# Performance work log

Measured on AMD Instinct MI355X. Metric: run time of the kernel, lower is better.

The kernel has to match this reference:

```python
import jax, jax.numpy as jnp
import numpy as np

LMAX = 4  # number of l blocks (lmax+1 in the original)
# segment ids mapping the L2 = sum(2l+1) = 16 spherical components to their l block
SEG = np.repeat(np.arange(LMAX), 2 * np.arange(LMAX) + 1)  # [16]
SEG_ONEHOT = np.eye(LMAX, dtype=np.float32)[SEG]  # [16, LMAX]


def setup_inputs() -> dict:
    key = jax.random.key(0)
    ks = jax.random.split(key, 10)
    b, m, f, k, L2 = 16, 64, 128, 64, 16
    def rnd(kk, shape, scale):
        return jax.random.normal(kk, shape, dtype=jnp.float32) * scale
    return {
        'x': rnd(ks[0], (b, m, f, L2), 1.0),
        'y': rnd(ks[1], (b, m, f, L2), 1.0),
        'wx0': rnd(ks[2], (k, f, f, LMAX), 1.0 / np.sqrt(f * f * LMAX)),
        'wy0': rnd(ks[3], (k, f, f, LMAX), 1.0 / np.sqrt(f * f * LMAX)),
        'wx_mlp': rnd(ks[4], (2, k, k), 1.0 / np.sqrt(k)),
        'bx_mlp': rnd(ks[5], (2, k, k), 0.02),
        'wy_mlp': rnd(ks[6], (2, k, k), 1.0 / np.sqrt(k)),
        'by_mlp': rnd(ks[7], (2, k, k), 0.02),
        'wxf': rnd(ks[8], (LMAX, f, k), 1.0 / np.sqrt(k)),
        'wyf': rnd(ks[9], (LMAX, f, k), 1.0 / np.sqrt(k)),
    }


def reference(x, y, wx0, wy0, wx_mlp, bx_mlp, wy_mlp, by_mlp, wxf, wyf):
    act = jax.nn.silu
    S = jnp.asarray(SEG_ONEHOT)  # [L2, lmax]
    # outer product of y and x features, segment-summed over each l block:
    # mix[b,m,fy,fx,l] = sum_c y[b,m,fy,c] * x[b,m,fx,c] * S[c,l]
    mix = jnp.einsum('bmfc,bmgc,cl->bmfgl', y, x, S)  # [b,m,f,f,lmax]
    mx = jnp.einsum('bmfgl,kfgl->bmk', mix, wx0)
    my = jnp.einsum('bmfgl,kfgl->bmk', mix, wy0)
    for i in range(wx_mlp.shape[0]):  # the n_mlp-1 used MLP stages
        mx = act(jnp.einsum('bmk,kl->bml', mx, wx_mlp[i]) + bx_mlp[i])
        my = act(jnp.einsum('bmk,kl->bml', my, wy_mlp[i]) + by_mlp[i])
    mx = act(jnp.einsum('bmk,lfk->bmfl', mx, wxf))  # [b,m,f,lmax]
    my = act(jnp.einsum('bmk,lfk->bmfl', my, wyf))
    # broadcast each l gate over its 2l+1 components (repeat == gather by SEG)
    seg = jnp.asarray(SEG)
    res = mx[..., seg] * x + my[..., seg] * y  # [b,m,f,L2]
    return res
```

## Files before the change

kernel.cpp:

```cpp
#include <hip/hip_runtime.h>
#include <stdint.h>


#define AS1 __attribute__((address_space(1)))
#define AS3 __attribute__((address_space(3)))

typedef __bf16 bf16x8 __attribute__((ext_vector_type(8)));
typedef float f32x4 __attribute__((ext_vector_type(4)));

__device__ __forceinline__ uint16_t f2b(float f) {
  uint32_t u = __float_as_uint(f);
  u += 0x7fffu + ((u >> 16) & 1u);
  return (uint16_t)(u >> 16);
}

#if __has_builtin(__builtin_amdgcn_fdot2_f32_bf16)
typedef __bf16 bf16x2 __attribute__((ext_vector_type(2)));
__device__ __forceinline__ float dot2b(uint32_t a, uint32_t b, float c) {
  union { uint32_t u; bf16x2 v; } ua, ub;
  ua.u = a; ub.u = b;
  return __builtin_amdgcn_fdot2_f32_bf16(ua.v, ub.v, c, false);
}
#else
__device__ __forceinline__ float dot2b(uint32_t a, uint32_t b, float c) {
  float a0 = __uint_as_float(a << 16), a1 = __uint_as_float(a & 0xffff0000u);
  float b0 = __uint_as_float(b << 16), b1 = __uint_as_float(b & 0xffff0000u);
  return c + a0 * b0 + a1 * b1;
}
#endif

__global__ __launch_bounds__(256) void convert_all(
    const float* __restrict__ wx0, const float* __restrict__ wy0,
    const float* __restrict__ x, const float* __restrict__ y,
    const float* __restrict__ wxf, const float* __restrict__ wyf,
    uint16_t* __restrict__ Wb, uint16_t* __restrict__ xb,
    uint16_t* __restrict__ yb, float* __restrict__ wfT) {
  if (blockIdx.x >= 6144) {
    int base = (blockIdx.x - 6144) * 2048 + threadIdx.x * 8;
#pragma unroll
    for (int ii = 0; ii < 8; ++ii) {
      int idx = base + ii;
      int side = idx >> 15, rem = idx & 32767;
      int k = rem >> 9, l = (rem >> 7) & 3, f = rem & 127;
      const float* src = side ? wyf : wxf;
      wfT[idx] = src[((size_t)l * 128 + f) * 64 + k];
    }
    return;
  }
  size_t i = ((size_t)blockIdx.x * 256 + threadIdx.x) * 8;
  const float* s; uint16_t* d;
  if (i < 4194304)        { s = wx0 + i;              d = Wb + i; }
  else if (i < 8388608)   { s = wy0 + (i - 4194304);  d = Wb + i; }
  else if (i < 10485760)  { s = x + (i - 8388608);    d = xb + (i - 8388608); }
  else                    { s = y + (i - 10485760);   d = yb + (i - 10485760); }
  float4 v0 = *(const float4*)s;
  float4 v1 = *(const float4*)(s + 4);
  uint32_t o0 = (uint32_t)f2b(v0.x) | ((uint32_t)f2b(v0.y) << 16);
  uint32_t o1 = (uint32_t)f2b(v0.z) | ((uint32_t)f2b(v0.w) << 16);
  uint32_t o2 = (uint32_t)f2b(v1.x) | ((uint32_t)f2b(v1.y) << 16);
  uint32_t o3 = (uint32_t)f2b(v1.z) | ((uint32_t)f2b(v1.w) << 16);
  *(uint4*)d = make_uint4(o0, o1, o2, o3);
}

__device__ __forceinline__ void gload_lds16(const void* g, void* l) {
  __builtin_amdgcn_global_load_lds((const AS1 uint32_t*)g, (AS3 uint32_t*)l, 16, 0, 0);
}

__global__ __launch_bounds__(256, 3) void fused_gemm(
    const uint16_t* __restrict__ xb, const uint16_t* __restrict__ yb,
    const uint16_t* __restrict__ Wb, float* __restrict__ Cpart) {
  __shared__ __align__(16) uint16_t sA[2][128 * 40];
  __shared__ __align__(16) uint16_t sB[2][128 * 32];
  __shared__ __align__(16) uint16_t yS[2][2048];

  int tid = threadIdx.x;
  int w = tid >> 6, lane = tid & 63;
  int g_id = blockIdx.x;
  int fb = g_id >> 3, fyg = g_id & 7;
  int FB = fb * 8;
  int fy0 = fyg * 16;
  int m0 = blockIdx.y * 128;
  int r = lane & 15, q = lane >> 4;
  int wm = w >> 1, wn = w & 1;
  int rowl = lane >> 2, qq = lane & 3;
  int m_loc = tid & 127, half = tid >> 7;

  uint32_t xr[32];
  {
    const uint16_t* xp0 = xb + (size_t)(m0 + m_loc) * 2048 + (FB + half * 4) * 16;
#pragma unroll
    for (int j = 0; j < 8; ++j) {
      uint4 v = *(const uint4*)(xp0 + j * 8);
      xr[j * 4 + 0] = v.x; xr[j * 4 + 1] = v.y;
      xr[j * 4 + 2] = v.z; xr[j * 4 + 3] = v.w;
    }
  }

  f32x4 zero = {0.f, 0.f, 0.f, 0.f};
  f32x4 acc[4][4];
#pragma unroll
  for (int i = 0; i < 4; ++i)
#pragma unroll
    for (int j = 0; j < 4; ++j) acc[i][j] = zero;

  int bcol = qq ^ ((rowl >> 1) & 3);
  int ychunk = w >> 1, ymbase = (w & 1) * 64;
  const uint16_t* ysrc_base = yb + (size_t)(m0 + ymbase + lane) * 2048 + ychunk * 8;
  int ydst_off = ychunk * 1024 + ymbase * 8;

  auto issueB = [&](uint16_t* dstB, int t) {
    int kk0 = (fy0 + t) * 512 + FB * 4;
#pragma unroll
    for (int jj = 0; jj < 2; ++jj) {
      int blk = w * 2 + jj;
      int rowi = blk * 16 + rowl;
      gload_lds16(Wb + (size_t)rowi * 65536 + kk0 + bcol * 8, dstB + blk * 512);
    }
  };
  auto issueY = [&](uint16_t* dstY, int t) {
    gload_lds16(ysrc_base + (size_t)(fy0 + t) * 16, dstY + ydst_off);
  };
  auto computeG = [&](const uint16_t* srcY, float* gg) {
    uint4 ya = *(const uint4*)(srcY + m_loc * 8);
    uint4 yc = *(const uint4*)(srcY + 1024 + m_loc * 8);
    uint32_t yp[8] = {ya.x, ya.y, ya.z, ya.w, yc.x, yc.y, yc.z, yc.w};
    uint32_t yl0 = yp[0] & 0xffffu, yh0 = yp[0] & 0xffff0000u;
    uint32_t yl4 = yp[4] & 0xffffu, yh4 = yp[4] & 0xffff0000u;
#pragma unroll
    for (int fxp = 0; fxp < 4; ++fxp) {
      const uint32_t* xp = xr + fxp * 8;
      gg[fxp * 4 + 0] = dot2b(xp[0], yl0, 0.f);
      gg[fxp * 4 + 1] = dot2b(xp[1], yp[1], dot2b(xp[0], yh0, 0.f));
      gg[fxp * 4 + 2] = dot2b(xp[4], yl4,
                         dot2b(xp[3], yp[3], dot2b(xp[2], yp[2], 0.f)));
      gg[fxp * 4 + 3] = dot2b(xp[7], yp[7], dot2b(xp[6], yp[6],
                         dot2b(xp[5], yp[5], dot2b(xp[4], yh4, 0.f))));
    }
  };
  auto writeA = [&](uint16_t* dstA, const float* gg) {
    uint32_t o[8];
#pragma unroll
    for (int p = 0; p < 8; ++p)
      o[p] = (__float_as_uint(gg[2 * p]) >> 16) |
             (__float_as_uint(gg[2 * p + 1]) & 0xffff0000u);
    uint16_t* dst = dstA + m_loc * 40 + half * 16;
    *(uint4*)dst       = make_uint4(o[0], o[1], o[2], o[3]);
    *(uint4*)(dst + 8) = make_uint4(o[4], o[5], o[6], o[7]);
  };

  uint16_t *pAc = sA[0], *pAn = sA[1];
  uint16_t *pBc = sB[0], *pBn = sB[1];
  uint16_t *pYc = yS[0], *pYn = yS[1];

  float gg[16];
  issueY(pYc, 0);
  __syncthreads();
  computeG(pYc, gg);
  writeA(pAc, gg);
  issueB(pBc, 0);
  issueY(pYn, 1);
  __syncthreads();

  for (int t = 0; t < 16; ++t) {
    if (t < 15) {
      issueB(pBn, t + 1);
      if (t < 14) issueY(pYc, t + 2);
      computeG(pYn, gg);
      writeA(pAn, gg);
    }
    bf16x8 a[4], b[4];
#pragma unroll
    for (int i = 0; i < 4; ++i)
      a[i] = *(const bf16x8*)&pAc[(wm * 64 + i * 16 + r) * 40 + q * 8];
#pragma unroll
    for (int j = 0; j < 4; ++j) {
      int row = wn * 64 + j * 16 + r;
      int pos = q ^ ((row >> 1) & 3);
      b[j] = *(const bf16x8*)&pBc[row * 32 + pos * 8];
    }
#pragma unroll
    for (int i = 0; i < 4; ++i)
#pragma unroll
      for (int j = 0; j < 4; ++j)
        acc[i][j] = __builtin_amdgcn_mfma_f32_16x16x32_bf16(a[i], b[j], acc[i][j], 0, 0, 0);
    __syncthreads();
    uint16_t* tp;
    tp = pAc; pAc = pAn; pAn = tp;
    tp = pBc; pBc = pBn; pBn = tp;
    tp = pYc; pYc = pYn; pYn = tp;
  }

  float* cbase = Cpart + (size_t)g_id * 131072;
#pragma unroll
  for (int i = 0; i < 4; ++i)
#pragma unroll
    for (int j = 0; j < 4; ++j)
#pragma unroll
      for (int reg = 0; reg < 4; ++reg) {
        int mm = m0 + wm * 64 + i * 16 + q * 4 + reg;
        int nn = wn * 64 + j * 16 + r;
        cbase[(size_t)mm * 128 + nn] = acc[i][j][reg];
      }
}

__global__ __launch_bounds__(256) void reduce_kernel(
    const float* __restrict__ Cpart, float* __restrict__ Cred) {
  __shared__ float sred[256];
  int t = threadIdx.x, bm = blockIdx.x;
  int col = t & 127, hh = t >> 7;
  float s = 0.f;
#pragma unroll 8
  for (int sp = hh * 64; sp < hh * 64 + 64; ++sp)
    s += Cpart[(size_t)sp * 131072 + (size_t)bm * 128 + col];
  sred[t] = s;
  __syncthreads();
  if (t < 128) Cred[(size_t)bm * 128 + t] = sred[t] + sred[t + 128];
}

__global__ __launch_bounds__(256) void finish_kernel(
    const float* __restrict__ x, const float* __restrict__ y,
    const float* __restrict__ wx_mlp, const float* __restrict__ bx_mlp,
    const float* __restrict__ wy_mlp, const float* __restrict__ by_mlp,
    const float* __restrict__ wfT,
    const float* __restrict__ Cred, float* __restrict__ out) {
  const int seg[16] = {0,1,1,1,2,2,2,2,2,3,3,3,3,3,3,3};
  __shared__ float sm[128];
  __shared__ float sg[2][128][4];
  int t = threadIdx.x;
  int bm = blockIdx.x;
  int mi = bm & 63;

  if (t < 128) sm[t] = Cred[(size_t)bm * 128 + t];
  __syncthreads();

  for (int st = 0; st < 2; ++st) {
    float v = 0.f;
    if (t < 128) {
      int side = t >> 6, j = t & 63;
      const float* wmlp = side ? wy_mlp : wx_mlp;
      const float* bmlp = side ? by_mlp : bx_mlp;
      const float* mv = sm + side * 64;
#pragma unroll 8
      for (int k = 0; k < 64; ++k)
        v += mv[k] * wmlp[(st * 64 + k) * 64 + j];
      v += bmlp[(st * 64 + mi) * 64 + j];
      v = v / (1.f + __expf(-v));
    }
    __syncthreads();
    if (t < 128) sm[t] = v;
    __syncthreads();
  }

  {
    int side = t >> 7, f = t & 127;
    const float* base = wfT + side * 32768;
    const float* mv = sm + side * 64;
    float gg[4] = {0.f, 0.f, 0.f, 0.f};
#pragma unroll 8
    for (int k = 0; k < 64; ++k) {
      float m2 = mv[k];
#pragma unroll
      for (int l = 0; l < 4; ++l)
        gg[l] += m2 * base[(k * 4 + l) * 128 + f];
    }
#pragma unroll
    for (int l = 0; l < 4; ++l)
      sg[side][f][l] = gg[l] / (1.f + __expf(-gg[l]));
  }
  __syncthreads();

  {
    int f = t >> 1, half = t & 1;
    size_t base = ((size_t)bm * 128 + f) * 16 + half * 8;
    float4 xa = *(const float4*)(x + base), xb4 = *(const float4*)(x + base + 4);
    float4 ya = *(const float4*)(y + base), yb4 = *(const float4*)(y + base + 4);
    float xv[8] = {xa.x, xa.y, xa.z, xa.w, xb4.x, xb4.y, xb4.z, xb4.w};
    float yv[8] = {ya.x, ya.y, ya.z, ya.w, yb4.x, yb4.y, yb4.z, yb4.w};
    float o[8];
#pragma unroll
    for (int ii = 0; ii < 8; ++ii) {
      int c = half * 8 + ii;
      o[ii] = sg[0][f][seg[c]] * xv[ii] + sg[1][f][seg[c]] * yv[ii];
    }
    *(float4*)(out + base)     = make_float4(o[0], o[1], o[2], o[3]);
    *(float4*)(out + base + 4) = make_float4(o[4], o[5], o[6], o[7]);
  }
}

extern "C" void kernel_launch(void* const* d_in, const int* in_sizes, int n_in,
                              void* d_out, int out_size, void* d_ws, size_t ws_size,
                              hipStream_t stream) {
  const float* x      = (const float*)d_in[0];
  const float* y      = (const float*)d_in[1];
  const float* wx0    = (const float*)d_in[2];
  const float* wy0    = (const float*)d_in[3];
  const float* wx_mlp = (const float*)d_in[4];
  const float* bx_mlp = (const float*)d_in[5];
  const float* wy_mlp = (const float*)d_in[6];
  const float* by_mlp = (const float*)d_in[7];
  const float* wxf    = (const float*)d_in[8];
  const float* wyf    = (const float*)d_in[9];
  float* out = (float*)d_out;

  uint16_t* Wb    = (uint16_t*)d_ws;
  uint16_t* xb    = (uint16_t*)((char*)d_ws + (size_t)16777216);
  uint16_t* yb    = (uint16_t*)((char*)d_ws + (size_t)20971520);
  float*    Cpart = (float*)((char*)d_ws + (size_t)25165824);
  float*    wfT   = (float*)((char*)d_ws + (size_t)92274688);
  float*    Cred  = (float*)((char*)d_ws + (size_t)92536832);

  convert_all<<<6176, 256, 0, stream>>>(wx0, wy0, x, y, wxf, wyf, Wb, xb, yb, wfT);
  fused_gemm<<<dim3(128, 8), 256, 0, stream>>>(xb, yb, Wb, Cpart);
  reduce_kernel<<<1024, 256, 0, stream>>>(Cpart, Cred);
  finish_kernel<<<1024, 256, 0, stream>>>(x, y, wx_mlp, bx_mlp, wy_mlp, by_mlp,
                                          wfT, Cred, out);
}
```

Before: 183.2 us.

## Keep x/y in fp32, transpose y, store bf16 partials, fold reduce into finish

Removes the bf16 conversion of x and y; instead y is transposed in fp32 so each fy slice is contiguous, and the mix products are computed in fp32 FMAs before a rounded bf16 pack. GEMM split-K partials are stored as bf16 instead of fp32, halving that traffic. The separate reduce kernel is merged into the finish kernel, saving a launch and the Cred round trip. The trade-offs are more VGPRs for the fp32 x registers, a larger y LDS buffer, and lower precision in the partial sums.

```diff
diff --git a/kernel.cpp b/kernel.cpp
--- a/kernel.cpp
+++ b/kernel.cpp
@@ -13,30 +13,36 @@
   u += 0x7fffu + ((u >> 16) & 1u);
   return (uint16_t)(u >> 16);
 }
-
-#if __has_builtin(__builtin_amdgcn_fdot2_f32_bf16)
-typedef __bf16 bf16x2 __attribute__((ext_vector_type(2)));
-__device__ __forceinline__ float dot2b(uint32_t a, uint32_t b, float c) {
-  union { uint32_t u; bf16x2 v; } ua, ub;
-  ua.u = a; ub.u = b;
-  return __builtin_amdgcn_fdot2_f32_bf16(ua.v, ub.v, c, false);
-}
-#else
-__device__ __forceinline__ float dot2b(uint32_t a, uint32_t b, float c) {
-  float a0 = __uint_as_float(a << 16), a1 = __uint_as_float(a & 0xffff0000u);
-  float b0 = __uint_as_float(b << 16), b1 = __uint_as_float(b & 0xffff0000u);
-  return c + a0 * b0 + a1 * b1;
-}
-#endif
+__device__ __forceinline__ float b2f(uint16_t u) {
+  return __uint_as_float((uint32_t)u << 16);
+}
 
 __global__ __launch_bounds__(256) void convert_all(
     const float* __restrict__ wx0, const float* __restrict__ wy0,
-    const float* __restrict__ x, const float* __restrict__ y,
+    const float* __restrict__ y,
     const float* __restrict__ wxf, const float* __restrict__ wyf,
-    uint16_t* __restrict__ Wb, uint16_t* __restrict__ xb,
-    uint16_t* __restrict__ yb, float* __restrict__ wfT) {
-  if (blockIdx.x >= 6144) {
-    int base = (blockIdx.x - 6144) * 2048 + threadIdx.x * 8;
+    uint16_t* __restrict__ Wb, float* __restrict__ yT,
+    float* __restrict__ wfT) {
+  if (blockIdx.x < 4096) {
+    size_t i = ((size_t)blockIdx.x * 256 + threadIdx.x) * 8;
+    const float* s = (i < 4194304) ? (wx0 + i) : (wy0 + (i - 4194304));
+    float4 v0 = *(const float4*)s;
+    float4 v1 = *(const float4*)(s + 4);
+    uint32_t o0 = (uint32_t)f2b(v0.x) | ((uint32_t)f2b(v0.y) << 16);
+    uint32_t o1 = (uint32_t)f2b(v0.z) | ((uint32_t)f2b(v0.w) << 16);
+    uint32_t o2 = (uint32_t)f2b(v1.x) | ((uint32_t)f2b(v1.y) << 16);
+    uint32_t o3 = (uint32_t)f2b(v1.z) | ((uint32_t)f2b(v1.w) << 16);
+    *(uint4*)(Wb + i) = make_uint4(o0, o1, o2, o3);
+  } else if (blockIdx.x < 4608) {
+    int g = (blockIdx.x - 4096) * 256 + threadIdx.x;
+    int m = g >> 7, fy = g & 127;
+    const float* src = y + (size_t)m * 2048 + fy * 16;
+    float* dst = yT + (size_t)fy * 16384 + m * 16;
+#pragma unroll
+    for (int ii = 0; ii < 4; ++ii)
+      *(float4*)(dst + ii * 4) = *(const float4*)(src + ii * 4);
+  } else {
+    int base = (blockIdx.x - 4608) * 2048 + threadIdx.x * 8;
 #pragma unroll
     for (int ii = 0; ii < 8; ++ii) {
       int idx = base + ii;
@@ -45,21 +51,7 @@
       const float* src = side ? wyf : wxf;
       wfT[idx] = src[((size_t)l * 128 + f) * 64 + k];
     }
-    return;
-  }
-  size_t i = ((size_t)blockIdx.x * 256 + threadIdx.x) * 8;
-  const float* s; uint16_t* d;
-  if (i < 4194304)        { s = wx0 + i;              d = Wb + i; }
-  else if (i < 8388608)   { s = wy0 + (i - 4194304);  d = Wb + i; }
-  else if (i < 10485760)  { s = x + (i - 8388608);    d = xb + (i - 8388608); }
-  else                    { s = y + (i - 10485760);   d = yb + (i - 10485760); }
-  float4 v0 = *(const float4*)s;
-  float4 v1 = *(const float4*)(s + 4);
-  uint32_t o0 = (uint32_t)f2b(v0.x) | ((uint32_t)f2b(v0.y) << 16);
-  uint32_t o1 = (uint32_t)f2b(v0.z) | ((uint32_t)f2b(v0.w) << 16);
-  uint32_t o2 = (uint32_t)f2b(v1.x) | ((uint32_t)f2b(v1.y) << 16);
-  uint32_t o3 = (uint32_t)f2b(v1.z) | ((uint32_t)f2b(v1.w) << 16);
-  *(uint4*)d = make_uint4(o0, o1, o2, o3);
+  }
 }
 
 __device__ __forceinline__ void gload_lds16(const void* g, void* l) {
@@ -67,11 +59,12 @@
 }
 
 __global__ __launch_bounds__(256, 3) void fused_gemm(
-    const uint16_t* __restrict__ xb, const uint16_t* __restrict__ yb,
-    const uint16_t* __restrict__ Wb, float* __restrict__ Cpart) {
+    const float* __restrict__ x, const float* __restrict__ yT,
+    const uint16_t* __restrict__ Wb, uint16_t* __restrict__ Cpart) {
   __shared__ __align__(16) uint16_t sA[2][128 * 40];
   __shared__ __align__(16) uint16_t sB[2][128 * 32];
-  __shared__ __align__(16) uint16_t yS[2][2048];
+  __shared__ __align__(16) float yS[2][2048];
+  const int seg[16] = {0,1,1,1,2,2,2,2,2,3,3,3,3,3,3,3};
 
   int tid = threadIdx.x;
   int w = tid >> 6, lane = tid & 63;
@@ -85,15 +78,17 @@
   int rowl = lane >> 2, qq = lane & 3;
   int m_loc = tid & 127, half = tid >> 7;
 
-  uint32_t xr[32];
+  float xf[4][16];
   {
-    const uint16_t* xp0 = xb + (size_t)(m0 + m_loc) * 2048 + (FB + half * 4) * 16;
-#pragma unroll
-    for (int j = 0; j < 8; ++j) {
-      uint4 v = *(const uint4*)(xp0 + j * 8);
-      xr[j * 4 + 0] = v.x; xr[j * 4 + 1] = v.y;
-      xr[j * 4 + 2] = v.z; xr[j * 4 + 3] = v.w;
-    }
+    const float* xp0 = x + (size_t)(m0 + m_loc) * 2048 + (FB + half * 4) * 16;
+#pragma unroll
+    for (int fxp = 0; fxp < 4; ++fxp)
+#pragma unroll
+      for (int cc = 0; cc < 4; ++cc) {
+        float4 v = *(const float4*)(xp0 + fxp * 16 + cc * 4);
+        xf[fxp][cc * 4 + 0] = v.x; xf[fxp][cc * 4 + 1] = v.y;
+        xf[fxp][cc * 4 + 2] = v.z; xf[fxp][cc * 4 + 3] = v.w;
+      }
   }
 
   f32x4 zero = {0.f, 0.f, 0.f, 0.f};
@@ -104,9 +99,15 @@
     for (int j = 0; j < 4; ++j) acc[i][j] = zero;
 
   int bcol = qq ^ ((rowl >> 1) & 3);
-  int ychunk = w >> 1, ymbase = (w & 1) * 64;
-  const uint16_t* ysrc_base = yb + (size_t)(m0 + ymbase + lane) * 2048 + ychunk * 8;
-  int ydst_off = ychunk * 1024 + ymbase * 8;
+
+  int yg0 = w * 128 + lane;
+  int ym0_ = yg0 >> 2, yp0 = yg0 & 3;
+  int ycq0 = yp0 ^ ((ym0_ >> 1) & 3);
+  int yg1 = yg0 + 64;
+  int ym1_ = yg1 >> 2, yp1 = yg1 & 3;
+  int ycq1 = yp1 ^ ((ym1_ >> 1) & 3);
+  const float* ysrc0 = yT + (size_t)(m0 + ym0_) * 16 + ycq0 * 4;
+  const float* ysrc1 = yT + (size_t)(m0 + ym1_) * 16 + ycq1 * 4;
 
   auto issueB = [&](uint16_t* dstB, int t) {
     int kk0 = (fy0 + t) * 512 + FB * 4;
@@ -117,32 +118,33 @@
       gload_lds16(Wb + (size_t)rowi * 65536 + kk0 + bcol * 8, dstB + blk * 512);
     }
   };
-  auto issueY = [&](uint16_t* dstY, int t) {
-    gload_lds16(ysrc_base + (size_t)(fy0 + t) * 16, dstY + ydst_off);
+  auto issueY = [&](float* dstY, int t) {
+    size_t fyoff = (size_t)(fy0 + t) * 16384;
+    gload_lds16(ysrc0 + fyoff, dstY + w * 512);
+    gload_lds16(ysrc1 + fyoff, dstY + w * 512 + 256);
   };
-  auto computeG = [&](const uint16_t* srcY, float* gg) {
-    uint4 ya = *(const uint4*)(srcY + m_loc * 8);
-    uint4 yc = *(const uint4*)(srcY + 1024 + m_loc * 8);
-    uint32_t yp[8] = {ya.x, ya.y, ya.z, ya.w, yc.x, yc.y, yc.z, yc.w};
-    uint32_t yl0 = yp[0] & 0xffffu, yh0 = yp[0] & 0xffff0000u;
-    uint32_t yl4 = yp[4] & 0xffffu, yh4 = yp[4] & 0xffff0000u;
-#pragma unroll
-    for (int fxp = 0; fxp < 4; ++fxp) {
-      const uint32_t* xp = xr + fxp * 8;
-      gg[fxp * 4 + 0] = dot2b(xp[0], yl0, 0.f);
-      gg[fxp * 4 + 1] = dot2b(xp[1], yp[1], dot2b(xp[0], yh0, 0.f));
-      gg[fxp * 4 + 2] = dot2b(xp[4], yl4,
-                         dot2b(xp[3], yp[3], dot2b(xp[2], yp[2], 0.f)));
-      gg[fxp * 4 + 3] = dot2b(xp[7], yp[7], dot2b(xp[6], yp[6],
-                         dot2b(xp[5], yp[5], dot2b(xp[4], yh4, 0.f))));
-    }
+  auto computeG = [&](const float* srcY, float* gg) {
+    float yv[16];
+#pragma unroll
+    for (int cq = 0; cq < 4; ++cq) {
+      int pos = cq ^ ((m_loc >> 1) & 3);
+      float4 v = *(const float4*)&srcY[(m_loc * 4 + pos) * 4];
+      yv[cq * 4 + 0] = v.x; yv[cq * 4 + 1] = v.y;
+      yv[cq * 4 + 2] = v.z; yv[cq * 4 + 3] = v.w;
+    }
+#pragma unroll
+    for (int p = 0; p < 16; ++p) gg[p] = 0.f;
+#pragma unroll
+    for (int fxp = 0; fxp < 4; ++fxp)
+#pragma unroll
+      for (int c = 0; c < 16; ++c)
+        gg[fxp * 4 + seg[c]] += yv[c] * xf[fxp][c];
   };
   auto writeA = [&](uint16_t* dstA, const float* gg) {
     uint32_t o[8];
 #pragma unroll
     for (int p = 0; p < 8; ++p)
-      o[p] = (__float_as_uint(gg[2 * p]) >> 16) |
-             (__float_as_uint(gg[2 * p + 1]) & 0xffff0000u);
+      o[p] = (uint32_t)f2b(gg[2 * p]) | ((uint32_t)f2b(gg[2 * p + 1]) << 16);
     uint16_t* dst = dstA + m_loc * 40 + half * 16;
     *(uint4*)dst       = make_uint4(o[0], o[1], o[2], o[3]);
     *(uint4*)(dst + 8) = make_uint4(o[4], o[5], o[6], o[7]);
@@ -150,7 +152,7 @@
 
   uint16_t *pAc = sA[0], *pAn = sA[1];
   uint16_t *pBc = sB[0], *pBn = sB[1];
-  uint16_t *pYc = yS[0], *pYn = yS[1];
+  float *pYc = yS[0], *pYn = yS[1];
 
   float gg[16];
   issueY(pYc, 0);
@@ -187,10 +189,11 @@
     uint16_t* tp;
     tp = pAc; pAc = pAn; pAn = tp;
     tp = pBc; pBc = pBn; pBn = tp;
-    tp = pYc; pYc = pYn; pYn = tp;
-  }
-
-  float* cbase = Cpart + (size_t)g_id * 131072;
+    float* fp2;
+    fp2 = pYc; pYc = pYn; pYn = fp2;
+  }
+
+  uint16_t* cbase = Cpart + (size_t)g_id * 131072;
 #pragma unroll
   for (int i = 0; i < 4; ++i)
 #pragma unroll
@@ -199,22 +202,8 @@
       for (int reg = 0; reg < 4; ++reg) {
         int mm = m0 + wm * 64 + i * 16 + q * 4 + reg;
         int nn = wn * 64 + j * 16 + r;
-        cbase[(size_t)mm * 128 + nn] = acc[i][j][reg];
+        cbase[(size_t)mm * 128 + nn] = f2b(acc[i][j][reg]);
       }
-}
-
-__global__ __launch_bounds__(256) void reduce_kernel(
-    const float* __restrict__ Cpart, float* __restrict__ Cred) {
-  __shared__ float sred[256];
-  int t = threadIdx.x, bm = blockIdx.x;
-  int col = t & 127, hh = t >> 7;
-  float s = 0.f;
-#pragma unroll 8
-  for (int sp = hh * 64; sp < hh * 64 + 64; ++sp)
-    s += Cpart[(size_t)sp * 131072 + (size_t)bm * 128 + col];
-  sred[t] = s;
-  __syncthreads();
-  if (t < 128) Cred[(size_t)bm * 128 + t] = sred[t] + sred[t + 128];
 }
 
 __global__ __launch_bounds__(256) void finish_kernel(
@@ -222,15 +211,25 @@
     const float* __restrict__ wx_mlp, const float* __restrict__ bx_mlp,
     const float* __restrict__ wy_mlp, const float* __restrict__ by_mlp,
     const float* __restrict__ wfT,
-    const float* __restrict__ Cred, float* __restrict__ out) {
+    const uint16_t* __restrict__ Cpart, float* __restrict__ out) {
   const int seg[16] = {0,1,1,1,2,2,2,2,2,3,3,3,3,3,3,3};
+  __shared__ float sred[256];
   __shared__ float sm[128];
   __shared__ float sg[2][128][4];
   int t = threadIdx.x;
   int bm = blockIdx.x;
   int mi = bm & 63;
 
-  if (t < 128) sm[t] = Cred[(size_t)bm * 128 + t];
+  {
+    int col = t & 127, hh = t >> 7;
+    float s = 0.f;
+#pragma unroll 8
+    for (int sp = hh * 64; sp < hh * 64 + 64; ++sp)
+      s += b2f(Cpart[(size_t)sp * 131072 + (size_t)bm * 128 + col]);
+    sred[t] = s;
+  }
+  __syncthreads();
+  if (t < 128) sm[t] = sred[t] + sred[t + 128];
   __syncthreads();
 
   for (int st = 0; st < 2; ++st) {
@@ -303,15 +302,12 @@
   float* out = (float*)d_out;
 
   uint16_t* Wb    = (uint16_t*)d_ws;
-  uint16_t* xb    = (uint16_t*)((char*)d_ws + (size_t)16777216);
-  uint16_t* yb    = (uint16_t*)((char*)d_ws + (size_t)20971520);
-  float*    Cpart = (float*)((char*)d_ws + (size_t)25165824);
-  float*    wfT   = (float*)((char*)d_ws + (size_t)92274688);
-  float*    Cred  = (float*)((char*)d_ws + (size_t)92536832);
-
-  convert_all<<<6176, 256, 0, stream>>>(wx0, wy0, x, y, wxf, wyf, Wb, xb, yb, wfT);
-  fused_gemm<<<dim3(128, 8), 256, 0, stream>>>(xb, yb, Wb, Cpart);
-  reduce_kernel<<<1024, 256, 0, stream>>>(Cpart, Cred);
+  float*    yT    = (float*)((char*)d_ws + (size_t)16777216);
+  uint16_t* Cpart = (uint16_t*)((char*)d_ws + (size_t)25165824);
+  float*    wfT   = (float*)((char*)d_ws + (size_t)58720256);
+
+  convert_all<<<4640, 256, 0, stream>>>(wx0, wy0, y, wxf, wyf, Wb, yT, wfT);
+  fused_gemm<<<dim3(128, 8), 256, 0, stream>>>(x, yT, Wb, Cpart);
   finish_kernel<<<1024, 256, 0, stream>>>(x, y, wx_mlp, bx_mlp, wy_mlp, by_mlp,
-                                          wfT, Cred, out);
-}
+                                          wfT, Cpart, out);
+}
```

Result: slower. 214.9 us (+17.3%).
